# Performance work log

Hardware: AMD Instinct MI355X
Metric: run time of the kernel (lower is better)

The kernel has to match this reference:

```python
import jax, jax.numpy as jnp
import numpy as np

EPS = 1e-5
DIL = 1
PAD = 1
STRIDE = 1

def conv2d(x, w, stride=1, pad=1, dil=1):
    return jax.lax.conv_general_dilated(x, w, (stride, stride), [(pad, pad), (pad, pad)],
                                        rhs_dilation=(dil, dil),
                                        dimension_numbers=('NCHW', 'OIHW', 'NCHW'))

def batchnorm(x, g, b, m, v):
    inv = g / jnp.sqrt(v + EPS)
    return x * inv[None, :, None, None] + (b - m * inv)[None, :, None, None]

def _bilinear(img, y, x):
    # img: [C,H,W]; y,x: [Ho,Wo] float sample coords; zero padding outside.
    H, W = img.shape[1], img.shape[2]
    y0 = jnp.floor(y); x0 = jnp.floor(x)
    ty = y - y0; tx = x - x0
    y0i = y0.astype(jnp.int32); x0i = x0.astype(jnp.int32)
    def g(yi, xi):
        valid = (yi >= 0) & (yi < H) & (xi >= 0) & (xi < W)
        v = img[:, jnp.clip(yi, 0, H - 1), jnp.clip(xi, 0, W - 1)]  # [C,Ho,Wo]
        return jnp.where(valid[None], v, jnp.zeros((), img.dtype))
    return (g(y0i, x0i) * ((1 - ty) * (1 - tx))[None]
            + g(y0i, x0i + 1) * ((1 - ty) * tx)[None]
            + g(y0i + 1, x0i) * (ty * (1 - tx))[None]
            + g(y0i + 1, x0i + 1) * (ty * tx)[None])

def deform_conv(x, w, offset, stride=1, pad=1, dil=1):
    # offset: [B, 18, Ho, Wo], channels 0:9 = dy per kernel tap (row-major), 9:18 = dx.
    B, C, H, W = x.shape
    Co = w.shape[0]
    Ho = (H + 2 * pad - dil * 2 - 1) // stride + 1
    Wo = (W + 2 * pad - dil * 2 - 1) // stride + 1
    off = offset.reshape(B, 2, 9, Ho, Wo)
    iy = (jnp.arange(Ho) * stride - pad).astype(x.dtype)
    ix = (jnp.arange(Wo) * stride - pad).astype(x.dtype)
    wk = w.reshape(Co, C, 9)
    out = jnp.zeros((B, Co, Ho, Wo), x.dtype)
    for k in range(9):  # fixed 3x3 kernel taps
        ky, kx = k // 3, k % 3
        ys = iy[:, None] + ky * dil + off[:, 0, k]  # [B,Ho,Wo]
        xs = ix[None, :] + kx * dil + off[:, 1, k]
        val = jax.vmap(_bilinear)(x, ys, xs)        # [B,C,Ho,Wo]
        out = out + jnp.einsum('bchw,oc->bohw', val, wk[:, :, k])
    return out

def offset_bias(dil, dtype):
    bw = jnp.array([[-1., 0., 1.]] * 3, dtype) * (dil - 1)
    bh = bw.T
    return jnp.concatenate([bh.reshape(-1), bw.reshape(-1)])  # [18]

def setup_inputs() -> dict:
    key = jax.random.key(0)
    ks = jax.random.split(key, 12)
    B, C, H, W = 8, 256, 56, 56
    inp = {
        'x': jax.random.normal(ks[0], (B, C, H, W), jnp.float32),
        'conv1_w': jax.random.normal(ks[1], (C, C, 3, 3), jnp.float32) * 0.02,
        'bn1_g': jax.random.normal(ks[2], (C,), jnp.float32) * 0.1 + 1.0,
        'bn1_b': jax.random.normal(ks[3], (C,), jnp.float32) * 0.1,
        'bn1_m': jax.random.normal(ks[4], (C,), jnp.float32) * 0.1,
        'bn1_v': jax.random.uniform(ks[5], (C,), jnp.float32) + 0.5,
        'off_w': jax.random.normal(ks[6], (18, C, 3, 3), jnp.float32) * 0.01,
        'off_b': jnp.zeros((18,), jnp.float32),
        'conv2_w': jax.random.normal(ks[7], (C, C, 3, 3), jnp.float32) * 0.02,
        'bn2_g': jax.random.normal(ks[8], (C,), jnp.float32) * 0.1 + 1.0,
        'bn2_b': jax.random.normal(ks[9], (C,), jnp.float32) * 0.1,
        'bn2_m': jax.random.normal(ks[10], (C,), jnp.float32) * 0.1,
        'bn2_v': jax.random.uniform(ks[11], (C,), jnp.float32) + 0.5,
    }
    return inp

def reference(x, conv1_w, bn1_g, bn1_b, bn1_m, bn1_v, off_w, off_b, conv2_w, bn2_g, bn2_b, bn2_m, bn2_v):
    residual = x
    out = conv2d(x, conv1_w, STRIDE, PAD, DIL)
    out = jax.nn.relu(batchnorm(out, bn1_g, bn1_b, bn1_m, bn1_v))
    offset = conv2d(out, off_w, STRIDE, PAD, DIL) + off_b[None, :, None, None]
    offset = offset + offset_bias(DIL, out.dtype)[None, :, None, None]
    out = deform_conv(out, conv2_w, offset, STRIDE, PAD, DIL)
    out = batchnorm(out, bn2_g, bn2_b, bn2_m, bn2_v)
    return jax.nn.relu(out + residual)
```

## Files before the change

### kernel.cpp

```cpp
#include <hip/hip_runtime.h>

#define NB 8
#define NH 56
#define NW 56
#define NHW 3136
#define NCHW 802816
#define NPIX 25088
#define NHP 58
#define EPSV 1e-5f

typedef float f32x4 __attribute__((ext_vector_type(4)));
typedef __bf16 bf16x8 __attribute__((ext_vector_type(8)));

__device__ __forceinline__ unsigned short f2b(float f) {
  unsigned int u = __float_as_uint(f);
  u += 0x7FFFu + ((u >> 16) & 1u);
  return (unsigned short)(u >> 16);
}
__device__ __forceinline__ float blo(unsigned int u){ return __uint_as_float(u << 16); }
__device__ __forceinline__ float bhi(unsigned int u){ return __uint_as_float(u & 0xFFFF0000u); }
__device__ __forceinline__ unsigned int pack_trunc(float f0, float f1) {
  return __builtin_amdgcn_perm(__float_as_uint(f1), __float_as_uint(f0), 0x07060302u);
}
__device__ __forceinline__ bf16x8 asbf(const uint4& q) { return *(const bf16x8*)&q; }

__global__ __launch_bounds__(256) void clear_borders(
    unsigned short* __restrict__ xbp, unsigned short* __restrict__ t1b)
{
  int i = blockIdx.x*256 + threadIdx.x;
  int q = i & 31; int pid = i >> 5;
  int b = pid / 228, j = pid % 228;
  int y, x;
  if (j < 58)       { y = 0;  x = j; }
  else if (j < 116) { y = 57; x = j - 58; }
  else { int jj = j - 116; y = 1 + (jj >> 1); x = (jj & 1) * 57; }
  size_t addr = ((size_t)(b*NHP + y)*NHP + x)*256 + q*8;
  uint4 z = make_uint4(0u,0u,0u,0u);
  *(uint4*)(xbp + addr) = z;
  *(uint4*)(t1b + addr) = z;
}

__global__ __launch_bounds__(256) void prep_x(
    const float* __restrict__ x, unsigned short* __restrict__ xbp)
{
  __shared__ float T[64][65];
  const int pxt  = blockIdx.x * 64;
  const int cg   = blockIdx.y * 64;
  const int b    = pxt / NHW;
  const int rem0 = pxt % NHW;
  const int t    = threadIdx.x;
  const int pl   = t & 63;
  const int c0   = t >> 6;
  const float* src = x + (size_t)b*NCHW + rem0;
  #pragma unroll
  for (int it = 0; it < 16; ++it) {
    int c = c0 + it*4;
    T[c][pl] = src[(size_t)(cg + c)*NHW + pl];
  }
  __syncthreads();
  const int pr = t >> 5;
  const int cp = t & 31;
  #pragma unroll
  for (int it = 0; it < 8; ++it) {
    int pxl = pr + it*8;
    int rem = rem0 + pxl;
    int ho = rem / NW, wo = rem % NW;
    unsigned int pk = ((unsigned int)f2b(T[cp*2+1][pxl]) << 16) | (unsigned int)f2b(T[cp*2][pxl]);
    *(unsigned int*)(xbp + ((size_t)(b*NHP + ho + 1)*NHP + (wo + 1))*256 + cg + cp*2) = pk;
  }
}

__global__ __launch_bounds__(256) void prep_wq(
    const float* __restrict__ w, unsigned short* __restrict__ wq)
{
  int i = blockIdx.x*256 + threadIdx.x;
  int j  = i & 7;
  int n  = (i >> 3) & 255;
  int kc = (i >> 11) & 7;
  int r  = i >> 14;
  int ktap = r >> 2, cic = r & 3;
  int ci = cic*64 + kc*8 + j;
  wq[i] = f2b(w[((size_t)n*256 + ci)*9 + ktap]);
}

__global__ __launch_bounds__(256) void prep_wq3(
    const float* __restrict__ ow, unsigned short* __restrict__ wq)
{
  int i = blockIdx.x*256 + threadIdx.x;
  int j  = i & 7;
  int n  = (i >> 3) & 31;
  int kc = (i >> 8) & 7;
  int r  = i >> 11;
  int ktap = r >> 2, cic = r & 3;
  int ci = cic*64 + kc*8 + j;
  wq[i] = (n < 18) ? f2b(ow[((size_t)n*256 + ci)*9 + ktap]) : (unsigned short)0;
}

__device__ __forceinline__ int tapoff(int r) {
  int k = r >> 2, cic = r & 3;
  int ky = k/3, kx = k - ky*3;
  return (ky*NHP + kx)*256 + cic*64;
}

__global__ __launch_bounds__(512, 4) void gemm_conv1(
    const unsigned short* __restrict__ xbp, const unsigned short* __restrict__ w1q,
    const float* __restrict__ gam, const float* __restrict__ bet,
    const float* __restrict__ mu,  const float* __restrict__ var,
    unsigned short* __restrict__ t1b)
{
  __shared__ unsigned short SMEM[18432];
  unsigned short* Al = SMEM;

  const int m0   = blockIdx.x * 64;
  const int t    = threadIdx.x;
  const int lane = t & 63;
  const int wv   = t >> 6;
  const int wvM  = wv & 1;
  const int wvN  = wv >> 1;
  const int quad = lane >> 4;
  const int l15  = lane & 15;

  const int srow = t >> 3, seg = t & 7, sxor = srow & 7;
  const int px = m0 + srow;
  const int b = px / NHW, rem = px % NHW;
  const int ho = rem / NW, wo = rem % NW;
  const unsigned int pbase = ((unsigned int)(b*NHP + ho)*NHP + wo)*256u + seg*8u;

  const unsigned short* bqb = w1q + (size_t)(wvN*64 + l15)*8;
#define BQ1(R,KK,NT) (const uint4*)(bqb + ((size_t)(((R)*8 + (KK)*4 + quad))*256 + (NT)*16)*8)

  f32x4 acc[2][4];
  #pragma unroll
  for (int i = 0; i < 2; ++i)
    #pragma unroll
    for (int j = 0; j < 4; ++j) acc[i][j] = (f32x4)(0.f);

  uint4 pb0[4];
  {
    uint4 pA = *(const uint4*)(xbp + pbase + tapoff(0));
    #pragma unroll
    for (int nt = 0; nt < 4; ++nt) pb0[nt] = *BQ1(0,0,nt);
    *(uint4*)(&Al[srow*64 + ((seg ^ sxor)*8)]) = pA;
    __syncthreads();
  }

  for (int r = 0; r < 36; ++r) {
    const int cur = (r & 1) * 4096;
    const int nxt = 4096 - cur;
    const int rn  = (r < 35) ? r + 1 : 35;
    uint4 pAn = *(const uint4*)(xbp + pbase + tapoff(rn));
    uint4 pb1[4];
    #pragma unroll
    for (int nt = 0; nt < 4; ++nt) pb1[nt] = *BQ1(r,1,nt);
    __builtin_amdgcn_sched_barrier(0);
    {
      const int s8 = quad ^ (l15 & 7);
      bf16x8 af0 = *(const bf16x8*)(&Al[cur + (wvM*32 +      l15)*64 + s8*8]);
      bf16x8 af1 = *(const bf16x8*)(&Al[cur + (wvM*32 + 16 + l15)*64 + s8*8]);
      #pragma unroll
      for (int nt = 0; nt < 4; ++nt) {
        bf16x8 bv = asbf(pb0[nt]);
        acc[0][nt] = __builtin_amdgcn_mfma_f32_16x16x32_bf16(af0, bv, acc[0][nt], 0, 0, 0);
        acc[1][nt] = __builtin_amdgcn_mfma_f32_16x16x32_bf16(af1, bv, acc[1][nt], 0, 0, 0);
      }
    }
    #pragma unroll
    for (int nt = 0; nt < 4; ++nt) pb0[nt] = *BQ1(rn,0,nt);
    __builtin_amdgcn_sched_barrier(0);
    {
      const int s8 = (4 + quad) ^ (l15 & 7);
      bf16x8 af0 = *(const bf16x8*)(&Al[cur + (wvM*32 +      l15)*64 + s8*8]);
      bf16x8 af1 = *(const bf16x8*)(&Al[cur + (wvM*32 + 16 + l15)*64 + s8*8]);
      #pragma unroll
      for (int nt = 0; nt < 4; ++nt) {
        bf16x8 bv = asbf(pb1[nt]);
        acc[0][nt] = __builtin_amdgcn_mfma_f32_16x16x32_bf16(af0, bv, acc[0][nt], 0, 0, 0);
        acc[1][nt] = __builtin_amdgcn_mfma_f32_16x16x32_bf16(af1, bv, acc[1][nt], 0, 0, 0);
      }
    }
    *(uint4*)(&Al[nxt + srow*64 + ((seg ^ sxor)*8)]) = pAn;
    __syncthreads();
  }
#undef BQ1

  unsigned short* Sw = SMEM + wv*2304;
  #pragma unroll
  for (int nt = 0; nt < 4; ++nt) {
    const int co = wvN*64 + nt*16 + l15;
    const float inv  = gam[co] * rsqrtf(var[co] + EPSV);
    const float beta = bet[co] - mu[co]*inv;
    #pragma unroll
    for (int mt = 0; mt < 2; ++mt) {
      #pragma unroll
      for (int rr = 0; rr < 4; ++rr) {
        const int pxl = mt*16 + quad*4 + rr;
        float val = acc[mt][nt][rr]*inv + beta;
        val = val > 0.f ? val : 0.f;
        Sw[pxl*72 + nt*16 + l15] = f2b(val);
      }
    }
  }
  __builtin_amdgcn_s_waitcnt(0xC07F);
  __builtin_amdgcn_s_barrier();
  #pragma unroll
  for (int i = 0; i < 4; ++i) {
    const int pxl = (lane >> 3) + 8*i;
    const int sc  = lane & 7;
    uint4 q = *(const uint4*)(&Sw[pxl*72 + sc*8]);
    const int pg = m0 + wvM*32 + pxl;
    const int bb = pg / NHW, rm = pg % NHW;
    const int hh = rm / NW, ww = rm % NW;
    *(uint4*)(t1b + ((size_t)(bb*NHP + hh + 1)*NHP + ww + 1)*256 + wvN*64 + sc*8) = q;
  }
}

__global__ __launch_bounds__(256, 6) void gemm_off(
    const unsigned short* __restrict__ t1b, const unsigned short* __restrict__ w3q,
    const float* __restrict__ ob, float* __restrict__ toff)
{
  __shared__ unsigned short Al[2*4096];

  const int m0 = blockIdx.x * 64;
  const int kc = blockIdx.y;
  const int t    = threadIdx.x;
  const int lane = t & 63;
  const int wv   = t >> 6;
  const int quad = lane >> 4;
  const int l15  = lane & 15;

  const int arow = t >> 2, as4 = t & 3, axor = arow & 7;
  const int pxa = m0 + arow;
  const int ba = pxa / NHW, rema = pxa % NHW;
  const unsigned int pbase = ((unsigned int)(ba*NHP + rema/NW)*NHP + rema%NW)*256u;

  const unsigned short* bqb = w3q + (size_t)l15*8;
#define BQ3(R,KK,NT) (const uint4*)(bqb + ((size_t)(((R)*8 + (KK)*4 + quad))*32 + (NT)*16)*8)

  f32x4 acc[2];
  #pragma unroll
  for (int nt = 0; nt < 2; ++nt) {
    float init = 0.f;
    if (kc == 0) { int co = nt*16 + l15; init = (co < 18) ? ob[co] : 0.f; }
    acc[nt] = (f32x4)(init);
  }

  uint4 pb0[2];
  {
    const int r0 = kc*9;
    uint4 pA0 = *(const uint4*)(t1b + pbase + tapoff(r0) + as4*8);
    uint4 pA1 = *(const uint4*)(t1b + pbase + tapoff(r0) + (as4+4)*8);
    #pragma unroll
    for (int nt = 0; nt < 2; ++nt) pb0[nt] = *BQ3(r0,0,nt);
    *(uint4*)(&Al[arow*64 + ((as4     ^ axor)*8)]) = pA0;
    *(uint4*)(&Al[arow*64 + (((as4+4) ^ axor)*8)]) = pA1;
    __syncthreads();
  }

  for (int rr = 0; rr < 9; ++rr) {
    const int r   = kc*9 + rr;
    const int cur = (rr & 1) * 4096;
    const int nxt = 4096 - cur;
    const int rn  = (rr < 8) ? r + 1 : r;
    uint4 pA0 = *(const uint4*)(t1b + pbase + tapoff(rn) + as4*8);
    uint4 pA1 = *(const uint4*)(t1b + pbase + tapoff(rn) + (as4+4)*8);
    uint4 pb1[2];
    #pragma unroll
    for (int nt = 0; nt < 2; ++nt) pb1[nt] = *BQ3(r,1,nt);
    __builtin_amdgcn_sched_barrier(0);
    {
      const int s8 = quad ^ (l15 & 7);
      bf16x8 af = *(const bf16x8*)(&Al[cur + (wv*16 + l15)*64 + s8*8]);
      #pragma unroll
      for (int nt = 0; nt < 2; ++nt)
        acc[nt] = __builtin_amdgcn_mfma_f32_16x16x32_bf16(af, asbf(pb0[nt]), acc[nt], 0, 0, 0);
    }
    #pragma unroll
    for (int nt = 0; nt < 2; ++nt) pb0[nt] = *BQ3(rn,0,nt);
    __builtin_amdgcn_sched_barrier(0);
    {
      const int s8 = (4 + quad) ^ (l15 & 7);
      bf16x8 af = *(const bf16x8*)(&Al[cur + (wv*16 + l15)*64 + s8*8]);
      #pragma unroll
      for (int nt = 0; nt < 2; ++nt)
        acc[nt] = __builtin_amdgcn_mfma_f32_16x16x32_bf16(af, asbf(pb1[nt]), acc[nt], 0, 0, 0);
    }
    *(uint4*)(&Al[nxt + arow*64 + ((as4     ^ axor)*8)]) = pA0;
    *(uint4*)(&Al[nxt + arow*64 + (((as4+4) ^ axor)*8)]) = pA1;
    __syncthreads();
  }
#undef BQ3

  #pragma unroll
  for (int nt = 0; nt < 2; ++nt) {
    const int co = nt*16 + l15;
    if (co < 18) {
      #pragma unroll
      for (int rr2 = 0; rr2 < 4; ++rr2) {
        const int pg = m0 + wv*16 + quad*4 + rr2;
        const int bb = pg / NHW, rm = pg % NHW;
        atomicAdd(&toff[(size_t)bb*(18*NHW) + (size_t)co*NHW + rm], acc[nt][rr2]);
      }
    }
  }
}

__global__ __launch_bounds__(512, 4) void gemm_deform(
    const unsigned short* __restrict__ t1b, const unsigned short* __restrict__ w2q,
    const float* __restrict__ toff, const float* __restrict__ xres,
    const float* __restrict__ gam, const float* __restrict__ bet,
    const float* __restrict__ mu,  const float* __restrict__ var,
    float* __restrict__ outp)
{
  __shared__ float SMEMF[8448];
  unsigned short* Al = (unsigned short*)SMEMF;

  const int m0   = blockIdx.x * 64;
  const int t    = threadIdx.x;
  const int lane = t & 63;
  const int wv   = t >> 6;
  const int wvM  = wv & 1;
  const int wvN  = wv >> 1;
  const int quad = lane >> 4;
  const int l15  = lane & 15;

  const int srow = t >> 3, seg = t & 7, sxor = srow & 7;
  const int px = m0 + srow;
  const int b = px / NHW, rem = px % NHW;
  const int ho = rem / NW, wo = rem % NW;
  const int obb = b*(18*NHW) + rem;
  const unsigned int prowb = (unsigned int)(b*NHP);

  const unsigned short* bqb = w2q + (size_t)(wvN*64 + l15)*8;
#define BQ2(R,KK,NT) (const uint4*)(bqb + ((size_t)(((R)*8 + (KK)*4 + quad))*256 + (NT)*16)*8)

  f32x4 acc[2][4];
  #pragma unroll
  for (int i = 0; i < 2; ++i)
    #pragma unroll
    for (int j = 0; j < 4; ++j) acc[i][j] = (f32x4)(0.f);

  unsigned int o00, o01, o10, o11;
  float w00, w01, w10, w11;
#define COORDS(KK) {                                                   \
    const int ky_ = (KK)/3, kx_ = (KK) - ky_*3;                        \
    const float offy = toff[obb + (KK)*NHW];                           \
    const float offx = toff[obb + (9+(KK))*NHW];                       \
    const float yf = (float)(ho - 1 + ky_) + offy;                     \
    const float xf = (float)(wo - 1 + kx_) + offx;                     \
    const float y0f = floorf(yf), x0f = floorf(xf);                    \
    const float ty = yf - y0f,   tx = xf - x0f;                        \
    const int y0p = (int)y0f + 1, x0p = (int)x0f + 1;                  \
    const int cy0 = min(max(y0p,   0), NHP-1);                         \
    const int cy1 = min(max(y0p+1, 0), NHP-1);                         \
    const int cx0 = min(max(x0p,   0), NHP-1);                         \
    const int cx1 = min(max(x0p+1, 0), NHP-1);                         \
    w00 = (1.f-ty)*(1.f-tx);  w01 = (1.f-ty)*tx;                       \
    w10 = ty*(1.f-tx);        w11 = ty*tx;                             \
    o00 = ((prowb + cy0)*NHP + cx0)*256u + seg*8u;                     \
    o01 = ((prowb + cy0)*NHP + cx1)*256u + seg*8u;                     \
    o10 = ((prowb + cy1)*NHP + cx0)*256u + seg*8u;                     \
    o11 = ((prowb + cy1)*NHP + cx1)*256u + seg*8u;                     \
  }
#define BILIN(RES, C00, C01, C10, C11) {                                             \
    uint4 res_;                                                                      \
    { float a0 = w00*blo(C00.x)+w01*blo(C01.x)+w10*blo(C10.x)+w11*blo(C11.x);        \
      float a1 = w00*bhi(C00.x)+w01*bhi(C01.x)+w10*bhi(C10.x)+w11*bhi(C11.x);        \
      res_.x = pack_trunc(a0, a1); }                                                 \
    { float a0 = w00*blo(C00.y)+w01*blo(C01.y)+w10*blo(C10.y)+w11*blo(C11.y);        \
      float a1 = w00*bhi(C00.y)+w01*bhi(C01.y)+w10*bhi(C10.y)+w11*bhi(C11.y);        \
      res_.y = pack_trunc(a0, a1); }                                                 \
    { float a0 = w00*blo(C00.z)+w01*blo(C01.z)+w10*blo(C10.z)+w11*blo(C11.z);        \
      float a1 = w00*bhi(C00.z)+w01*bhi(C01.z)+w10*bhi(C10.z)+w11*bhi(C11.z);        \
      res_.z = pack_trunc(a0, a1); }                                                 \
    { float a0 = w00*blo(C00.w)+w01*blo(C01.w)+w10*blo(C10.w)+w11*blo(C11.w);        \
      float a1 = w00*bhi(C00.w)+w01*bhi(C01.w)+w10*bhi(C10.w)+w11*bhi(C11.w);        \
      res_.w = pack_trunc(a0, a1); }                                                 \
    RES = res_;                                                                      \
  }

  uint4 pb0[4];
  {
    COORDS(0);
    uint4 c00 = *(const uint4*)(t1b + o00);
    uint4 c01 = *(const uint4*)(t1b + o01);
    uint4 c10 = *(const uint4*)(t1b + o10);
    uint4 c11 = *(const uint4*)(t1b + o11);
    #pragma unroll
    for (int nt = 0; nt < 4; ++nt) pb0[nt] = *BQ2(0,0,nt);
    uint4 res; BILIN(res, c00, c01, c10, c11);
    *(uint4*)(&Al[srow*64 + ((seg ^ sxor)*8)]) = res;
    __syncthreads();
  }

  for (int r = 0; r < 36; ++r) {
    const int cur = (r & 1) * 4096;
    const int nxt = 4096 - cur;
    const int rn  = (r < 35) ? r + 1 : 35;
    if ((r & 3) == 3 && r < 35) COORDS((r+1) >> 2);
    const unsigned int cioN = (unsigned int)((rn & 3)*64);
    uint4 c00 = *(const uint4*)(t1b + o00 + cioN);
    uint4 c01 = *(const uint4*)(t1b + o01 + cioN);
    uint4 c10 = *(const uint4*)(t1b + o10 + cioN);
    uint4 c11 = *(const uint4*)(t1b + o11 + cioN);
    uint4 pb1[4];
    #pragma unroll
    for (int nt = 0; nt < 4; ++nt) pb1[nt] = *BQ2(r,1,nt);
    __builtin_amdgcn_sched_barrier(0);
    {
      const int s8 = quad ^ (l15 & 7);
      bf16x8 af0 = *(const bf16x8*)(&Al[cur + (wvM*32 +      l15)*64 + s8*8]);
      bf16x8 af1 = *(const bf16x8*)(&Al[cur + (wvM*32 + 16 + l15)*64 + s8*8]);
      #pragma unroll
      for (int nt = 0; nt < 4; ++nt) {
        bf16x8 bv = asbf(pb0[nt]);
        acc[0][nt] = __builtin_amdgcn_mfma_f32_16x16x32_bf16(af0, bv, acc[0][nt], 0, 0, 0);
        acc[1][nt] = __builtin_amdgcn_mfma_f32_16x16x32_bf16(af1, bv, acc[1][nt], 0, 0, 0);
      }
    }
    #pragma unroll
    for (int nt = 0; nt < 4; ++nt) pb0[nt] = *BQ2(rn,0,nt);
    __builtin_amdgcn_sched_barrier(0);
    {
      const int s8 = (4 + quad) ^ (l15 & 7);
      bf16x8 af0 = *(const bf16x8*)(&Al[cur + (wvM*32 +      l15)*64 + s8*8]);
      bf16x8 af1 = *(const bf16x8*)(&Al[cur + (wvM*32 + 16 + l15)*64 + s8*8]);
      #pragma unroll
      for (int nt = 0; nt < 4; ++nt) {
        bf16x8 bv = asbf(pb1[nt]);
        acc[0][nt] = __builtin_amdgcn_mfma_f32_16x16x32_bf16(af0, bv, acc[0][nt], 0, 0, 0);
        acc[1][nt] = __builtin_amdgcn_mfma_f32_16x16x32_bf16(af1, bv, acc[1][nt], 0, 0, 0);
      }
    }
    {
      uint4 res; BILIN(res, c00, c01, c10, c11);
      *(uint4*)(&Al[nxt + srow*64 + ((seg ^ sxor)*8)]) = res;
    }
    __syncthreads();
  }
#undef BQ2
#undef COORDS
#undef BILIN

  float* Sl = SMEMF + wv*1056;
  const int pxl_r = lane & 31;
  const int csel  = lane >> 5;
  const int pg    = m0 + wvM*32 + pxl_r;
  const int bo    = pg / NHW, remo = pg % NHW;
  const size_t obase = (size_t)bo*NCHW + remo;
  #pragma unroll
  for (int h = 0; h < 2; ++h) {
    __syncthreads();
    #pragma unroll
    for (int nt2 = 0; nt2 < 2; ++nt2) {
      const int nt = h*2 + nt2;
      #pragma unroll
      for (int mt = 0; mt < 2; ++mt) {
        #pragma unroll
        for (int rr = 0; rr < 4; ++rr) {
          const int pxl = mt*16 + quad*4 + rr;
          Sl[pxl*33 + nt2*16 + l15] = acc[mt][nt][rr];
        }
      }
    }
    __builtin_amdgcn_s_waitcnt(0xC07F);
    __builtin_amdgcn_s_barrier();
    #pragma unroll
    for (int j = 0; j < 16; ++j) {
      const int col = csel*16 + j;
      const int co  = wvN*64 + h*32 + col;
      const float inv  = gam[co] * rsqrtf(var[co] + EPSV);
      const float beta = bet[co] - mu[co]*inv;
      const size_t off = obase + (size_t)co*NHW;
      float val = Sl[pxl_r*33 + col];
      float o = val*inv + beta + xres[off];
      outp[off] = o > 0.f ? o : 0.f;
    }
  }
}

extern "C" void kernel_launch(void* const* d_in, const int* in_sizes, int n_in,
                              void* d_out, int out_size, void* d_ws, size_t ws_size,
                              hipStream_t stream) {
  const float* x   = (const float*)d_in[0];
  const float* w1  = (const float*)d_in[1];
  const float* g1  = (const float*)d_in[2];
  const float* b1  = (const float*)d_in[3];
  const float* m1  = (const float*)d_in[4];
  const float* v1  = (const float*)d_in[5];
  const float* ow  = (const float*)d_in[6];
  const float* ob  = (const float*)d_in[7];
  const float* w2  = (const float*)d_in[8];
  const float* g2  = (const float*)d_in[9];
  const float* b2  = (const float*)d_in[10];
  const float* m2  = (const float*)d_in[11];
  const float* v2  = (const float*)d_in[12];
  float* out = (float*)d_out;

  const size_t PADSZ = (size_t)NB*NHP*NHP*256;
  unsigned short* xbp = (unsigned short*)d_ws;
  unsigned short* t1b = xbp + PADSZ;
  float*          tof = (float*)(t1b + PADSZ);
  unsigned short* w1q = (unsigned short*)(tof + (size_t)NB*18*NHW);
  unsigned short* w2q = w1q + (size_t)589824;
  unsigned short* w3q = w2q + (size_t)589824;

  clear_borders<<<228, 256, 0, stream>>>(xbp, t1b);
  dim3 gp(392, 4, 1);
  prep_x<<<gp, 256, 0, stream>>>(x, xbp);
  prep_wq<<<2304, 256, 0, stream>>>(w1, w1q);
  prep_wq<<<2304, 256, 0, stream>>>(w2, w2q);
  prep_wq3<<<288, 256, 0, stream>>>(ow, w3q);
  hipMemsetAsync(tof, 0, (size_t)NB*18*NHW*sizeof(float), stream);

  gemm_conv1<<<392, 512, 0, stream>>>(xbp, w1q, g1, b1, m1, v1, t1b);
  dim3 go(392, 4, 1);
  gemm_off<<<go, 256, 0, stream>>>(t1b, w3q, ob, tof);
  gemm_deform<<<392, 512, 0, stream>>>(t1b, w2q, tof, x, g2, b2, m2, v2, out);
}
```

Measured before the change: 264.3 us.

## Split output channels across two blocks in conv1 and deform GEMMs

gemm_conv1 and gemm_deform now run as 2×392 grids of 256-thread blocks, each computing 128 output channels for 64 pixels, instead of 392 blocks of 512 threads covering all 256 channels. Each thread now stages two A rows. The explicit weight prefetch across iterations and the sched_barriers are removed; both K-halves of weights are loaded inside the same iteration. The bilinear interpolation is rewritten with two-wide float vectors, aiming at packed FMA. The gain is more, smaller blocks for occupancy and load balance. The cost is that the A-tile gather, including the deformable bilinear sampling, is now repeated by both channel-half blocks, and weight-load latency is less hidden.

```diff
diff --git a/kernel.cpp b/kernel.cpp
--- a/kernel.cpp
+++ b/kernel.cpp
@@ -10,6 +10,7 @@
 #define EPSV 1e-5f
 
 typedef float f32x4 __attribute__((ext_vector_type(4)));
+typedef float f32x2 __attribute__((ext_vector_type(2)));
 typedef __bf16 bf16x8 __attribute__((ext_vector_type(8)));
 
 __device__ __forceinline__ unsigned short f2b(float f) {
@@ -23,6 +24,9 @@
   return __builtin_amdgcn_perm(__float_as_uint(f1), __float_as_uint(f0), 0x07060302u);
 }
 __device__ __forceinline__ bf16x8 asbf(const uint4& q) { return *(const bf16x8*)&q; }
+__device__ __forceinline__ f32x2 up2(unsigned int u) {
+  f32x2 v; v.x = blo(u); v.y = bhi(u); return v;
+}
 
 __global__ __launch_bounds__(256) void clear_borders(
     unsigned short* __restrict__ xbp, unsigned short* __restrict__ t1b)
@@ -102,16 +106,17 @@
   return (ky*NHP + kx)*256 + cic*64;
 }
 
-__global__ __launch_bounds__(512, 4) void gemm_conv1(
+__global__ __launch_bounds__(256, 4) void gemm_conv1(
     const unsigned short* __restrict__ xbp, const unsigned short* __restrict__ w1q,
     const float* __restrict__ gam, const float* __restrict__ bet,
     const float* __restrict__ mu,  const float* __restrict__ var,
     unsigned short* __restrict__ t1b)
 {
-  __shared__ unsigned short SMEM[18432];
+  __shared__ unsigned short SMEM[9216];
   unsigned short* Al = SMEM;
 
-  const int m0   = blockIdx.x * 64;
+  const int n0   = blockIdx.x * 128;
+  const int m0   = blockIdx.y * 64;
   const int t    = threadIdx.x;
   const int lane = t & 63;
   const int wv   = t >> 6;
@@ -120,14 +125,17 @@
   const int quad = lane >> 4;
   const int l15  = lane & 15;
 
-  const int srow = t >> 3, seg = t & 7, sxor = srow & 7;
-  const int px = m0 + srow;
-  const int b = px / NHW, rem = px % NHW;
-  const int ho = rem / NW, wo = rem % NW;
-  const unsigned int pbase = ((unsigned int)(b*NHP + ho)*NHP + wo)*256u + seg*8u;
-
-  const unsigned short* bqb = w1q + (size_t)(wvN*64 + l15)*8;
-#define BQ1(R,KK,NT) (const uint4*)(bqb + ((size_t)(((R)*8 + (KK)*4 + quad))*256 + (NT)*16)*8)
+  const int srow = t >> 3, seg = t & 7;
+  unsigned int pbase[2];
+  #pragma unroll
+  for (int u = 0; u < 2; ++u) {
+    const int px = m0 + srow + 32*u;
+    const int b = px / NHW, rem = px % NHW;
+    pbase[u] = ((unsigned int)(b*NHP + rem/NW)*NHP + rem%NW)*256u + seg*8u;
+  }
+
+  const unsigned short* bqb = w1q + (size_t)(n0 + wvN*64 + l15)*8;
+#define BQ1(R,KK,NT) (const uint4*)(bqb + ((size_t)((R)*8 + (KK)*4 + quad))*2048 + (size_t)(NT)*128)
 
   f32x4 acc[2][4];
   #pragma unroll
@@ -135,12 +143,13 @@
     #pragma unroll
     for (int j = 0; j < 4; ++j) acc[i][j] = (f32x4)(0.f);
 
-  uint4 pb0[4];
   {
-    uint4 pA = *(const uint4*)(xbp + pbase + tapoff(0));
-    #pragma unroll
-    for (int nt = 0; nt < 4; ++nt) pb0[nt] = *BQ1(0,0,nt);
-    *(uint4*)(&Al[srow*64 + ((seg ^ sxor)*8)]) = pA;
+    #pragma unroll
+    for (int u = 0; u < 2; ++u) {
+      uint4 q = *(const uint4*)(xbp + pbase[u] + tapoff(0));
+      const int row = srow + 32*u;
+      *(uint4*)(&Al[row*64 + ((seg ^ (row & 7))*8)]) = q;
+    }
     __syncthreads();
   }
 
@@ -148,37 +157,30 @@
     const int cur = (r & 1) * 4096;
     const int nxt = 4096 - cur;
     const int rn  = (r < 35) ? r + 1 : 35;
-    uint4 pAn = *(const uint4*)(xbp + pbase + tapoff(rn));
-    uint4 pb1[4];
+    uint4 pA0 = *(const uint4*)(xbp + pbase[0] + tapoff(rn));
+    uint4 pA1 = *(const uint4*)(xbp + pbase[1] + tapoff(rn));
+    uint4 pb0[4], pb1[4];
+    #pragma unroll
+    for (int nt = 0; nt < 4; ++nt) pb0[nt] = *BQ1(r,0,nt);
     #pragma unroll
     for (int nt = 0; nt < 4; ++nt) pb1[nt] = *BQ1(r,1,nt);
-    __builtin_amdgcn_sched_barrier(0);
-    {
-      const int s8 = quad ^ (l15 & 7);
+    #pragma unroll
+    for (int kk = 0; kk < 2; ++kk) {
+      const int s8 = (kk*4 + quad) ^ (l15 & 7);
       bf16x8 af0 = *(const bf16x8*)(&Al[cur + (wvM*32 +      l15)*64 + s8*8]);
       bf16x8 af1 = *(const bf16x8*)(&Al[cur + (wvM*32 + 16 + l15)*64 + s8*8]);
       #pragma unroll
       for (int nt = 0; nt < 4; ++nt) {
-        bf16x8 bv = asbf(pb0[nt]);
+        bf16x8 bv = asbf(kk ? pb1[nt] : pb0[nt]);
         acc[0][nt] = __builtin_amdgcn_mfma_f32_16x16x32_bf16(af0, bv, acc[0][nt], 0, 0, 0);
         acc[1][nt] = __builtin_amdgcn_mfma_f32_16x16x32_bf16(af1, bv, acc[1][nt], 0, 0, 0);
       }
     }
-    #pragma unroll
-    for (int nt = 0; nt < 4; ++nt) pb0[nt] = *BQ1(rn,0,nt);
-    __builtin_amdgcn_sched_barrier(0);
     {
-      const int s8 = (4 + quad) ^ (l15 & 7);
-      bf16x8 af0 = *(const bf16x8*)(&Al[cur + (wvM*32 +      l15)*64 + s8*8]);
-      bf16x8 af1 = *(const bf16x8*)(&Al[cur + (wvM*32 + 16 + l15)*64 + s8*8]);
-      #pragma unroll
-      for (int nt = 0; nt < 4; ++nt) {
-        bf16x8 bv = asbf(pb1[nt]);
-        acc[0][nt] = __builtin_amdgcn_mfma_f32_16x16x32_bf16(af0, bv, acc[0][nt], 0, 0, 0);
-        acc[1][nt] = __builtin_amdgcn_mfma_f32_16x16x32_bf16(af1, bv, acc[1][nt], 0, 0, 0);
-      }
-    }
-    *(uint4*)(&Al[nxt + srow*64 + ((seg ^ sxor)*8)]) = pAn;
+      const int row0 = srow, row1 = srow + 32;
+      *(uint4*)(&Al[nxt + row0*64 + ((seg ^ (row0 & 7))*8)]) = pA0;
+      *(uint4*)(&Al[nxt + row1*64 + ((seg ^ (row1 & 7))*8)]) = pA1;
+    }
     __syncthreads();
   }
 #undef BQ1
@@ -186,7 +188,7 @@
   unsigned short* Sw = SMEM + wv*2304;
   #pragma unroll
   for (int nt = 0; nt < 4; ++nt) {
-    const int co = wvN*64 + nt*16 + l15;
+    const int co = n0 + wvN*64 + nt*16 + l15;
     const float inv  = gam[co] * rsqrtf(var[co] + EPSV);
     const float beta = bet[co] - mu[co]*inv;
     #pragma unroll
@@ -210,7 +212,7 @@
     const int pg = m0 + wvM*32 + pxl;
     const int bb = pg / NHW, rm = pg % NHW;
     const int hh = rm / NW, ww = rm % NW;
-    *(uint4*)(t1b + ((size_t)(bb*NHP + hh + 1)*NHP + ww + 1)*256 + wvN*64 + sc*8) = q;
+    *(uint4*)(t1b + ((size_t)(bb*NHP + hh + 1)*NHP + ww + 1)*256 + n0 + wvN*64 + sc*8) = q;
   }
 }
 
@@ -234,7 +236,7 @@
   const unsigned int pbase = ((unsigned int)(ba*NHP + rema/NW)*NHP + rema%NW)*256u;
 
   const unsigned short* bqb = w3q + (size_t)l15*8;
-#define BQ3(R,KK,NT) (const uint4*)(bqb + ((size_t)(((R)*8 + (KK)*4 + quad))*32 + (NT)*16)*8)
+#define BQ3(R,KK,NT) (const uint4*)(bqb + ((size_t)((R)*8 + (KK)*4 + quad))*256 + (size_t)(NT)*128)
 
   f32x4 acc[2];
   #pragma unroll
@@ -244,13 +246,10 @@
     acc[nt] = (f32x4)(init);
   }
 
-  uint4 pb0[2];
   {
     const int r0 = kc*9;
     uint4 pA0 = *(const uint4*)(t1b + pbase + tapoff(r0) + as4*8);
     uint4 pA1 = *(const uint4*)(t1b + pbase + tapoff(r0) + (as4+4)*8);
-    #pragma unroll
-    for (int nt = 0; nt < 2; ++nt) pb0[nt] = *BQ3(r0,0,nt);
     *(uint4*)(&Al[arow*64 + ((as4     ^ axor)*8)]) = pA0;
     *(uint4*)(&Al[arow*64 + (((as4+4) ^ axor)*8)]) = pA1;
     __syncthreads();
@@ -263,10 +262,11 @@
     const int rn  = (rr < 8) ? r + 1 : r;
     uint4 pA0 = *(const uint4*)(t1b + pbase + tapoff(rn) + as4*8);
     uint4 pA1 = *(const uint4*)(t1b + pbase + tapoff(rn) + (as4+4)*8);
-    uint4 pb1[2];
+    uint4 pb0[2], pb1[2];
+    #pragma unroll
+    for (int nt = 0; nt < 2; ++nt) pb0[nt] = *BQ3(r,0,nt);
     #pragma unroll
     for (int nt = 0; nt < 2; ++nt) pb1[nt] = *BQ3(r,1,nt);
-    __builtin_amdgcn_sched_barrier(0);
     {
       const int s8 = quad ^ (l15 & 7);
       bf16x8 af = *(const bf16x8*)(&Al[cur + (wv*16 + l15)*64 + s8*8]);
@@ -274,9 +274,6 @@
       for (int nt = 0; nt < 2; ++nt)
         acc[nt] = __builtin_amdgcn_mfma_f32_16x16x32_bf16(af, asbf(pb0[nt]), acc[nt], 0, 0, 0);
     }
-    #pragma unroll
-    for (int nt = 0; nt < 2; ++nt) pb0[nt] = *BQ3(rn,0,nt);
-    __builtin_amdgcn_sched_barrier(0);
     {
       const int s8 = (4 + quad) ^ (l15 & 7);
       bf16x8 af = *(const bf16x8*)(&Al[cur + (wv*16 + l15)*64 + s8*8]);
@@ -304,17 +301,18 @@
   }
 }
 
-__global__ __launch_bounds__(512, 4) void gemm_deform(
+__global__ __launch_bounds__(256, 4) void gemm_deform(
     const unsigned short* __restrict__ t1b, const unsigned short* __restrict__ w2q,
     const float* __restrict__ toff, const float* __restrict__ xres,
     const float* __restrict__ gam, const float* __restrict__ bet,
     const float* __restrict__ mu,  const float* __restrict__ var,
     float* __restrict__ outp)
 {
-  __shared__ float SMEMF[8448];
+  __shared__ float SMEMF[4224];
   unsigned short* Al = (unsigned short*)SMEMF;
 
-  const int m0   = blockIdx.x * 64;
+  const int n0   = blockIdx.x * 128;
+  const int m0   = blockIdx.y * 64;
   const int t    = threadIdx.x;
   const int lane = t & 63;
   const int wv   = t >> 6;
@@ -323,15 +321,19 @@
   const int quad = lane >> 4;
   const int l15  = lane & 15;
 
-  const int srow = t >> 3, seg = t & 7, sxor = srow & 7;
-  const int px = m0 + srow;
-  const int b = px / NHW, rem = px % NHW;
-  const int ho = rem / NW, wo = rem % NW;
-  const int obb = b*(18*NHW) + rem;
-  const unsigned int prowb = (unsigned int)(b*NHP);
-
-  const unsigned short* bqb = w2q + (size_t)(wvN*64 + l15)*8;
-#define BQ2(R,KK,NT) (const uint4*)(bqb + ((size_t)(((R)*8 + (KK)*4 + quad))*256 + (NT)*16)*8)
+  const int srow = t >> 3, seg = t & 7;
+  int obb[2]; unsigned int prowb[2]; int hoU[2], woU[2];
+  #pragma unroll
+  for (int u = 0; u < 2; ++u) {
+    const int px = m0 + srow + 32*u;
+    const int b = px / NHW, rem = px % NHW;
+    hoU[u] = rem / NW; woU[u] = rem % NW;
+    obb[u] = b*(18*NHW) + rem;
+    prowb[u] = (unsigned int)(b*NHP);
+  }
+
+  const unsigned short* bqb = w2q + (size_t)(n0 + wvN*64 + l15)*8;
+#define BQ2(R,KK,NT) (const uint4*)(bqb + ((size_t)((R)*8 + (KK)*4 + quad))*2048 + (size_t)(NT)*128)
 
   f32x4 acc[2][4];
   #pragma unroll
@@ -339,14 +341,14 @@
     #pragma unroll
     for (int j = 0; j < 4; ++j) acc[i][j] = (f32x4)(0.f);
 
-  unsigned int o00, o01, o10, o11;
-  float w00, w01, w10, w11;
-#define COORDS(KK) {                                                   \
+  unsigned int o00[2], o01[2], o10[2], o11[2];
+  float w00[2], w01[2], w10[2], w11[2];
+#define COORDS(KK) _Pragma("unroll") for (int u = 0; u < 2; ++u) {     \
     const int ky_ = (KK)/3, kx_ = (KK) - ky_*3;                        \
-    const float offy = toff[obb + (KK)*NHW];                           \
-    const float offx = toff[obb + (9+(KK))*NHW];                       \
-    const float yf = (float)(ho - 1 + ky_) + offy;                     \
-    const float xf = (float)(wo - 1 + kx_) + offx;                     \
+    const float offy = toff[obb[u] + (KK)*NHW];                        \
+    const float offx = toff[obb[u] + (9+(KK))*NHW];                    \
+    const float yf = (float)(hoU[u] - 1 + ky_) + offy;                 \
+    const float xf = (float)(woU[u] - 1 + kx_) + offx;                 \
     const float y0f = floorf(yf), x0f = floorf(xf);                    \
     const float ty = yf - y0f,   tx = xf - x0f;                        \
     const int y0p = (int)y0f + 1, x0p = (int)x0f + 1;                  \
@@ -354,41 +356,38 @@
     const int cy1 = min(max(y0p+1, 0), NHP-1);                         \
     const int cx0 = min(max(x0p,   0), NHP-1);                         \
     const int cx1 = min(max(x0p+1, 0), NHP-1);                         \
-    w00 = (1.f-ty)*(1.f-tx);  w01 = (1.f-ty)*tx;                       \
-    w10 = ty*(1.f-tx);        w11 = ty*tx;                             \
-    o00 = ((prowb + cy0)*NHP + cx0)*256u + seg*8u;                     \
-    o01 = ((prowb + cy0)*NHP + cx1)*256u + seg*8u;                     \
-    o10 = ((prowb + cy1)*NHP + cx0)*256u + seg*8u;                     \
-    o11 = ((prowb + cy1)*NHP + cx1)*256u + seg*8u;                     \
-  }
-#define BILIN(RES, C00, C01, C10, C11) {                                             \
-    uint4 res_;                                                                      \
-    { float a0 = w00*blo(C00.x)+w01*blo(C01.x)+w10*blo(C10.x)+w11*blo(C11.x);        \
-      float a1 = w00*bhi(C00.x)+w01*bhi(C01.x)+w10*bhi(C10.x)+w11*bhi(C11.x);        \
-      res_.x = pack_trunc(a0, a1); }                                                 \
-    { float a0 = w00*blo(C00.y)+w01*blo(C01.y)+w10*blo(C10.y)+w11*blo(C11.y);        \
-      float a1 = w00*bhi(C00.y)+w01*bhi(C01.y)+w10*bhi(C10.y)+w11*bhi(C11.y);        \
-      res_.y = pack_trunc(a0, a1); }                                                 \
-    { float a0 = w00*blo(C00.z)+w01*blo(C01.z)+w10*blo(C10.z)+w11*blo(C11.z);        \
-      float a1 = w00*bhi(C00.z)+w01*bhi(C01.z)+w10*bhi(C10.z)+w11*bhi(C11.z);        \
-      res_.z = pack_trunc(a0, a1); }                                                 \
-    { float a0 = w00*blo(C00.w)+w01*blo(C01.w)+w10*blo(C10.w)+w11*blo(C11.w);        \
-      float a1 = w00*bhi(C00.w)+w01*bhi(C01.w)+w10*bhi(C10.w)+w11*bhi(C11.w);        \
-      res_.w = pack_trunc(a0, a1); }                                                 \
-    RES = res_;                                                                      \
-  }
-
-  uint4 pb0[4];
+    w00[u] = (1.f-ty)*(1.f-tx);  w01[u] = (1.f-ty)*tx;                 \
+    w10[u] = ty*(1.f-tx);        w11[u] = ty*tx;                       \
+    o00[u] = ((prowb[u] + cy0)*NHP + cx0)*256u + seg*8u;               \
+    o01[u] = ((prowb[u] + cy0)*NHP + cx1)*256u + seg*8u;               \
+    o10[u] = ((prowb[u] + cy1)*NHP + cx0)*256u + seg*8u;               \
+    o11[u] = ((prowb[u] + cy1)*NHP + cx1)*256u + seg*8u;               \
+  }
+#define BLD(U, D, C00, C01, C10, C11)                                   \
+    ({ f32x2 r_ = up2(C00.D) * (f32x2)(w00[U]);                         \
+       r_ += up2(C01.D) * (f32x2)(w01[U]);                              \
+       r_ += up2(C10.D) * (f32x2)(w10[U]);                              \
+       r_ += up2(C11.D) * (f32x2)(w11[U]);                              \
+       pack_trunc(r_.x, r_.y); })
+#define BILIN(U, RES, C00, C01, C10, C11) {                             \
+    RES.x = BLD(U, x, C00, C01, C10, C11);                              \
+    RES.y = BLD(U, y, C00, C01, C10, C11);                              \
+    RES.z = BLD(U, z, C00, C01, C10, C11);                              \
+    RES.w = BLD(U, w, C00, C01, C10, C11);                              \
+  }
+
   {
     COORDS(0);
-    uint4 c00 = *(const uint4*)(t1b + o00);
-    uint4 c01 = *(const uint4*)(t1b + o01);
-    uint4 c10 = *(const uint4*)(t1b + o10);
-    uint4 c11 = *(const uint4*)(t1b + o11);
-    #pragma unroll
-    for (int nt = 0; nt < 4; ++nt) pb0[nt] = *BQ2(0,0,nt);
-    uint4 res; BILIN(res, c00, c01, c10, c11);
-    *(uint4*)(&Al[srow*64 + ((seg ^ sxor)*8)]) = res;
+    #pragma unroll
+    for (int u = 0; u < 2; ++u) {
+      uint4 c00 = *(const uint4*)(t1b + o00[u]);
+      uint4 c01 = *(const uint4*)(t1b + o01[u]);
+      uint4 c10 = *(const uint4*)(t1b + o10[u]);
+      uint4 c11 = *(const uint4*)(t1b + o11[u]);
+      uint4 res; BILIN(u, res, c00, c01, c10, c11);
+      const int row = srow + 32*u;
+      *(uint4*)(&Al[row*64 + ((seg ^ (row & 7))*8)]) = res;
+    }
     __syncthreads();
   }
 
@@ -398,48 +397,43 @@
     const int rn  = (r < 35) ? r + 1 : 35;
     if ((r & 3) == 3 && r < 35) COORDS((r+1) >> 2);
     const unsigned int cioN = (unsigned int)((rn & 3)*64);
-    uint4 c00 = *(const uint4*)(t1b + o00 + cioN);
-    uint4 c01 = *(const uint4*)(t1b + o01 + cioN);
-    uint4 c10 = *(const uint4*)(t1b + o10 + cioN);
-    uint4 c11 = *(const uint4*)(t1b + o11 + cioN);
-    uint4 pb1[4];
+    uint4 c00[2], c01[2], c10[2], c11[2];
+    #pragma unroll
+    for (int u = 0; u < 2; ++u) {
+      c00[u] = *(const uint4*)(t1b + o00[u] + cioN);
+      c01[u] = *(const uint4*)(t1b + o01[u] + cioN);
+      c10[u] = *(const uint4*)(t1b + o10[u] + cioN);
+      c11[u] = *(const uint4*)(t1b + o11[u] + cioN);
+    }
+    uint4 pb0[4], pb1[4];
+    #pragma unroll
+    for (int nt = 0; nt < 4; ++nt) pb0[nt] = *BQ2(r,0,nt);
     #pragma unroll
     for (int nt = 0; nt < 4; ++nt) pb1[nt] = *BQ2(r,1,nt);
-    __builtin_amdgcn_sched_barrier(0);
-    {
-      const int s8 = quad ^ (l15 & 7);
+    #pragma unroll
+    for (int kk = 0; kk < 2; ++kk) {
+      const int s8 = (kk*4 + quad) ^ (l15 & 7);
       bf16x8 af0 = *(const bf16x8*)(&Al[cur + (wvM*32 +      l15)*64 + s8*8]);
       bf16x8 af1 = *(const bf16x8*)(&Al[cur + (wvM*32 + 16 + l15)*64 + s8*8]);
       #pragma unroll
       for (int nt = 0; nt < 4; ++nt) {
-        bf16x8 bv = asbf(pb0[nt]);
+        bf16x8 bv = asbf(kk ? pb1[nt] : pb0[nt]);
         acc[0][nt] = __builtin_amdgcn_mfma_f32_16x16x32_bf16(af0, bv, acc[0][nt], 0, 0, 0);
         acc[1][nt] = __builtin_amdgcn_mfma_f32_16x16x32_bf16(af1, bv, acc[1][nt], 0, 0, 0);
       }
     }
     #pragma unroll
-    for (int nt = 0; nt < 4; ++nt) pb0[nt] = *BQ2(rn,0,nt);
-    __builtin_amdgcn_sched_barrier(0);
-    {
-      const int s8 = (4 + quad) ^ (l15 & 7);
-      bf16x8 af0 = *(const bf16x8*)(&Al[cur + (wvM*32 +      l15)*64 + s8*8]);
-      bf16x8 af1 = *(const bf16x8*)(&Al[cur + (wvM*32 + 16 + l15)*64 + s8*8]);
-      #pragma unroll
-      for (int nt = 0; nt < 4; ++nt) {
-        bf16x8 bv = asbf(pb1[nt]);
-        acc[0][nt] = __builtin_amdgcn_mfma_f32_16x16x32_bf16(af0, bv, acc[0][nt], 0, 0, 0);
-        acc[1][nt] = __builtin_amdgcn_mfma_f32_16x16x32_bf16(af1, bv, acc[1][nt], 0, 0, 0);
-      }
-    }
-    {
-      uint4 res; BILIN(res, c00, c01, c10, c11);
-      *(uint4*)(&Al[nxt + srow*64 + ((seg ^ sxor)*8)]) = res;
+    for (int u = 0; u < 2; ++u) {
+      uint4 res; BILIN(u, res, c00[u], c01[u], c10[u], c11[u]);
+      const int row = srow + 32*u;
+      *(uint4*)(&Al[nxt + row*64 + ((seg ^ (row & 7))*8)]) = res;
     }
     __syncthreads();
   }
 #undef BQ2
 #undef COORDS
 #undef BILIN
+#undef BLD
 
   float* Sl = SMEMF + wv*1056;
   const int pxl_r = lane & 31;
@@ -467,7 +461,7 @@
     #pragma unroll
     for (int j = 0; j < 16; ++j) {
       const int col = csel*16 + j;
-      const int co  = wvN*64 + h*32 + col;
+      const int co  = n0 + wvN*64 + h*32 + col;
       const float inv  = gam[co] * rsqrtf(var[co] + EPSV);
       const float beta = bet[co] - mu[co]*inv;
       const size_t off = obase + (size_t)co*NHW;
@@ -512,8 +506,9 @@
   prep_wq3<<<288, 256, 0, stream>>>(ow, w3q);
   hipMemsetAsync(tof, 0, (size_t)NB*18*NHW*sizeof(float), stream);
 
-  gemm_conv1<<<392, 512, 0, stream>>>(xbp, w1q, g1, b1, m1, v1, t1b);
+  dim3 gg(2, 392, 1);
+  gemm_conv1<<<gg, 256, 0, stream>>>(xbp, w1q, g1, b1, m1, v1, t1b);
   dim3 go(392, 4, 1);
   gemm_off<<<go, 256, 0, stream>>>(t1b, w3q, ob, tof);
-  gemm_deform<<<392, 512, 0, stream>>>(t1b, w2q, tof, x, g2, b2, m2, v2, out);
-}
+  gemm_deform<<<gg, 256, 0, stream>>>(t1b, w2q, tof, x, g2, b2, m2, v2, out);
+}
```

Result: slower. 305.5 us (+15.6%).
